# Optimization experiments

Measured on AMD Instinct MI355X. Metric: run time of the kernel, lower is better.

Reference implementation:

```python
import jax, jax.numpy as jnp
import numpy as np

D = 256
K = 64


def setup_inputs() -> dict:
    key = jax.random.key(0)
    k1, k2, k3 = jax.random.split(key, 3)
    B, H, W = 16, 96, 96
    X = jax.random.normal(k1, (B, D, H, W), dtype=jnp.float32)
    std1 = 1.0 / float(np.sqrt(K * D))
    std2 = 1.0 / float(np.sqrt(K))
    codewords = jax.random.uniform(k2, (K, D), dtype=jnp.float32, minval=-std1, maxval=std1)
    scale = jax.random.uniform(k3, (K,), dtype=jnp.float32, minval=-std2, maxval=std2)
    return {"X": X, "codewords": codewords, "scale": scale}


def reference(X, codewords, scale):
    # X: [B, D, H, W] -> Xf: [B, N, D]
    B = X.shape[0]
    Xf = X.reshape(B, X.shape[1], -1).transpose(0, 2, 1)
    # Scaled L2 distances: SL[b,n,k] = scale[k] * ||x_bn - c_k||^2
    x2 = jnp.sum(Xf * Xf, axis=-1, keepdims=True)          # [B, N, 1]
    c2 = jnp.sum(codewords * codewords, axis=-1)            # [K]
    xc = jnp.einsum('bnd,kd->bnk', Xf, codewords)           # [B, N, K]
    SL = scale * (x2 - 2.0 * xc + c2)                       # [B, N, K]
    # Assignment weights: softmax over codewords K
    A = jax.nn.softmax(SL, axis=-1)                         # [B, N, K]
    # Aggregate residuals: E[b,k,d] = sum_n A[b,n,k] * (X[b,n,d] - C[k,d])
    E = jnp.einsum('bnk,bnd->bkd', A, Xf) - jnp.sum(A, axis=1)[:, :, None] * codewords
    return E
```

## Files before the change

kernel.cpp:

```cpp
#include <hip/hip_runtime.h>

#define NDIM  256
#define NK    64
#define NPIX  9216
#define NB    16
#define TN    64
#define NW    48
#define TPB   3
#define GRID  (NB*NW)

typedef _Float16 half2_t __attribute__((ext_vector_type(2)));
typedef _Float16 half8_t __attribute__((ext_vector_type(8)));
typedef float    f32x4  __attribute__((ext_vector_type(4)));

__device__ __forceinline__ float fdot2(half2_t a, half2_t b, float c) {
  return __builtin_amdgcn_fdot2(a, b, c, false);
}

#define OFF_CH     0
#define OFF_C2     (NK * NDIM / 2)
#define OFF_ASUM   (OFF_C2 + NK)
#define OFF_APART  (OFF_ASUM + NB * NK)
#define OFF_EPART  (OFF_APART + GRID * NK)
#define WS_NEED    ((size_t)OFF_EPART * 4 + (size_t)GRID * NK * NDIM * 2)

__global__ void c2ch_kernel(const float* __restrict__ Cw, float* __restrict__ c2,
                            _Float16* __restrict__ ChH) {
  const int k = blockIdx.x, t = threadIdx.x;
  const float4 v = *(const float4*)(Cw + k * NDIM + 4 * t);
  half2_t h0; h0.x = (_Float16)v.x; h0.y = (_Float16)v.y;
  half2_t h1; h1.x = (_Float16)v.z; h1.y = (_Float16)v.w;
  *(half2_t*)&ChH[k * NDIM + 4 * t]     = h0;
  *(half2_t*)&ChH[k * NDIM + 4 * t + 2] = h1;
  float s = v.x*v.x + v.y*v.y + v.z*v.z + v.w*v.w;
#pragma unroll
  for (int o = 32; o; o >>= 1) s += __shfl_down(s, o);
  if (t == 0) c2[k] = s;
}

__global__ __launch_bounds__(256, 2) void encode_main(
    const float* __restrict__ X, const _Float16* __restrict__ ChH,
    const float* __restrict__ scale, const float* __restrict__ c2,
    void* __restrict__ Eout, float* __restrict__ Aout, int mode)
{
  __shared__ _Float16 XbS[32 * 66 * 8];
  __shared__ _Float16 Al[NK][72];
  __shared__ float red2[4][TN];
  __shared__ float redM[4][TN];
  __shared__ float redS[4][TN];

  const int tid  = threadIdx.x;
  const int w    = __builtin_amdgcn_readfirstlane(tid >> 6);
  const int lane = tid & 63;
  const int m    = lane & 15, quad = lane >> 4;
  const int b    = blockIdx.x / NW;
  const int wid  = blockIdx.x % NW;
  const float* Xbase = X + (size_t)b * NDIM * NPIX;
  const int kbase = w * 16;

  half8_t af1[8];
#pragma unroll
  for (int ks = 0; ks < 8; ++ks)
    af1[ks] = *(const half8_t*)(ChH + (kbase + m) * NDIM + ks * 32 + quad * 8);

  const float4 scv = *(const float4*)(scale + kbase + quad * 4);
  const float4 c2v = *(const float4*)(c2 + kbase + quad * 4);
  const float sc[4] = {scv.x, scv.y, scv.z, scv.w};
  const float sq[4] = {scv.x * c2v.x, scv.y * c2v.y, scv.z * c2v.z, scv.w * c2v.w};

  f32x4 acc_e[4][4];
#pragma unroll
  for (int i = 0; i < 4; ++i)
#pragma unroll
    for (int j = 0; j < 4; ++j)
      acc_e[i][j] = (f32x4){0.f, 0.f, 0.f, 0.f};
  float asum_acc = 0.f;

  float xv[64];
  {
    const float* Xg = Xbase + (size_t)(w * 64) * NPIX + wid * TN + lane;
#pragma unroll
    for (int i = 0; i < 64; ++i) xv[i] = Xg[(size_t)i * NPIX];
  }

  for (int tt = 0; tt < TPB; ++tt) {
    __syncthreads();

    {
      float xsq = 0.f;
#pragma unroll
      for (int g = 0; g < 8; ++g) {
        half8_t hv;
#pragma unroll
        for (int i = 0; i < 8; ++i) {
          const float v = xv[g * 8 + i];
          hv[i] = (_Float16)v; xsq += v * v;
        }
        *(half8_t*)&XbS[((w * 8 + g) * 66 + lane) * 8] = hv;
      }
      red2[w][lane] = xsq;
    }
    __syncthreads();

    if (tt + 1 < TPB) {
      const float* Xg = Xbase + (size_t)(w * 64) * NPIX + (wid + (tt + 1) * NW) * TN + lane;
#pragma unroll
      for (int i = 0; i < 64; ++i) xv[i] = Xg[(size_t)i * NPIX];
    }

    f32x4 accs[4];
#pragma unroll
    for (int nt = 0; nt < 4; ++nt) accs[nt] = (f32x4){0.f, 0.f, 0.f, 0.f};
#pragma unroll
    for (int ks = 0; ks < 8; ++ks) {
#pragma unroll
      for (int nt = 0; nt < 4; ++nt) {
        const half8_t bf = *(const half8_t*)&XbS[((ks * 4 + quad) * 66 + nt * 16 + m) * 8];
        accs[nt] = __builtin_amdgcn_mfma_f32_16x16x32_f16(af1[ks], bf, accs[nt], 0, 0, 0);
      }
    }

    float e[4][4], mw[4];
#pragma unroll
    for (int nt = 0; nt < 4; ++nt) {
      const int p = nt * 16 + m;
      const float x2p = red2[0][p] + red2[1][p] + red2[2][p] + red2[3][p];
      float L[4];
      float mx = -3.0e38f;
#pragma unroll
      for (int r = 0; r < 4; ++r) {
        L[r] = sc[r] * x2p - 2.f * sc[r] * accs[nt][r] + sq[r];
        mx = fmaxf(mx, L[r]);
      }
      mx = fmaxf(mx, __shfl_xor(mx, 16));
      mx = fmaxf(mx, __shfl_xor(mx, 32));
      float s = 0.f;
#pragma unroll
      for (int r = 0; r < 4; ++r) { e[nt][r] = __expf(L[r] - mx); s += e[nt][r]; }
      s += __shfl_xor(s, 16);
      s += __shfl_xor(s, 32);
      mw[nt] = mx;
      if (lane < 16) { redM[w][p] = mx; redS[w][p] = s; }
    }
    __syncthreads();
#pragma unroll
    for (int nt = 0; nt < 4; ++nt) {
      const int p = nt * 16 + m;
      const float M = fmaxf(fmaxf(redM[0][p], redM[1][p]),
                            fmaxf(redM[2][p], redM[3][p]));
      const float T = redS[0][p] * __expf(redM[0][p] - M)
                    + redS[1][p] * __expf(redM[1][p] - M)
                    + redS[2][p] * __expf(redM[2][p] - M)
                    + redS[3][p] * __expf(redM[3][p] - M);
      const float norm = __expf(mw[nt] - M) / T;
#pragma unroll
      for (int r = 0; r < 4; ++r)
        Al[kbase + quad * 4 + r][p] = (_Float16)(e[nt][r] * norm);
    }
    __syncthreads();

#pragma unroll
    for (int ks = 0; ks < 2; ++ks) {
      half8_t ba[4];
#pragma unroll
      for (int kt = 0; kt < 4; ++kt)
        ba[kt] = *(const half8_t*)&Al[kt * 16 + m][ks * 32 + quad * 8];
#pragma unroll
      for (int dt = 0; dt < 4; ++dt) {
        const int c = w * 8 + dt * 2 + (m >> 3);
        const int dlow = m & 7;
        half8_t xa;
#pragma unroll
        for (int j = 0; j < 8; ++j)
          xa[j] = XbS[(c * 66 + ks * 32 + quad * 8 + j) * 8 + dlow];
#pragma unroll
        for (int kt = 0; kt < 4; ++kt)
          acc_e[dt][kt] = __builtin_amdgcn_mfma_f32_16x16x32_f16(xa, ba[kt], acc_e[dt][kt], 0, 0, 0);
      }
    }
    if (tid < NK) {
      const half2_t one = {(_Float16)1.f, (_Float16)1.f};
#pragma unroll
      for (int lc = 0; lc < 8; ++lc) {
        const half8_t sv = *(const half8_t*)&Al[tid][lc * 8];
        asum_acc = fdot2(__builtin_shufflevector(sv, sv, 0, 1), one, asum_acc);
        asum_acc = fdot2(__builtin_shufflevector(sv, sv, 2, 3), one, asum_acc);
        asum_acc = fdot2(__builtin_shufflevector(sv, sv, 4, 5), one, asum_acc);
        asum_acc = fdot2(__builtin_shufflevector(sv, sv, 6, 7), one, asum_acc);
      }
    }
  }

  __syncthreads();
  _Float16* Et = XbS;
#pragma unroll
  for (int dt = 0; dt < 4; ++dt)
#pragma unroll
    for (int kt = 0; kt < 4; ++kt)
#pragma unroll
      for (int r = 0; r < 4; ++r) {
        const int k = kt * 16 + m;
        const int d = w * 64 + dt * 16 + quad * 4 + r;
        Et[k * 264 + d] = (_Float16)acc_e[dt][kt][r];
      }
  __syncthreads();
  const int ko = tid >> 2, cq = tid & 3;
  if (mode) {
    _Float16* Ebk = (_Float16*)Eout + (size_t)blockIdx.x * (NK * NDIM);
#pragma unroll
    for (int g = 0; g < 8; ++g)
      *(half8_t*)&Ebk[ko * NDIM + cq * 64 + g * 8] =
          *(const half8_t*)&Et[ko * 264 + cq * 64 + g * 8];
    if (tid < NK) Aout[blockIdx.x * NK + tid] = asum_acc;
  } else {
    float* Ebk = (float*)Eout + (size_t)b * (NK * NDIM);
#pragma unroll
    for (int g = 0; g < 64; ++g)
      atomicAdd(&Ebk[ko * NDIM + cq * 64 + g], (float)Et[ko * 264 + cq * 64 + g]);
    if (tid < NK) atomicAdd(&Aout[b * NK + tid], asum_acc);
  }
}

__global__ void asum_reduce_kernel(const float* __restrict__ Apart,
                                   float* __restrict__ asum) {
  const int i = blockIdx.x * 256 + threadIdx.x;
  const int bb = i >> 6, k = i & 63;
  float s = 0.f;
#pragma unroll 8
  for (int w = 0; w < NW; ++w) s += Apart[(bb * NW + w) * NK + k];
  asum[i] = s;
}

__global__ void finalize_partials(const _Float16* __restrict__ EpartH,
                                  const float* __restrict__ asum,
                                  const float* __restrict__ Cw,
                                  float* __restrict__ out) {
  const int g = blockIdx.x * 256 + threadIdx.x;
  const int i0 = g * 8;
  const int bb = i0 >> 14;
  const int o  = i0 & 16383;
  const int k  = o >> 8, d = i0 & 255;
  float s[8];
#pragma unroll
  for (int j = 0; j < 8; ++j) s[j] = 0.f;
  const _Float16* base = EpartH + (((size_t)bb * NW) << 14) + o;
#pragma unroll 4
  for (int w = 0; w < NW; ++w) {
    const half8_t v = *(const half8_t*)(base + ((size_t)w << 14));
#pragma unroll
    for (int j = 0; j < 8; ++j) s[j] += (float)v[j];
  }
  const float a = asum[bb * NK + k];
  const float4 c0 = *(const float4*)(Cw + k * NDIM + d);
  const float4 c1 = *(const float4*)(Cw + k * NDIM + d + 4);
  float4 r0, r1;
  r0.x = s[0] - a * c0.x; r0.y = s[1] - a * c0.y;
  r0.z = s[2] - a * c0.z; r0.w = s[3] - a * c0.w;
  r1.x = s[4] - a * c1.x; r1.y = s[5] - a * c1.y;
  r1.z = s[6] - a * c1.z; r1.w = s[7] - a * c1.w;
  *(float4*)(out + i0)     = r0;
  *(float4*)(out + i0 + 4) = r1;
}

__global__ void finalize_atomic(const float* __restrict__ E_acc,
                                const float* __restrict__ asum,
                                const float* __restrict__ Cw,
                                float* __restrict__ out) {
  const int i = blockIdx.x * 256 + threadIdx.x;
  const int d = i & 255;
  const int k = (i >> 8) & 63;
  const int bb = i >> 14;
  out[i] = E_acc[i] - asum[bb * NK + k] * Cw[k * NDIM + d];
}

extern "C" void kernel_launch(void* const* d_in, const int* in_sizes, int n_in,
                              void* d_out, int out_size, void* d_ws, size_t ws_size,
                              hipStream_t stream) {
  const float* X     = (const float*)d_in[0];
  const float* Cw    = (const float*)d_in[1];
  const float* scale = (const float*)d_in[2];
  float* out = (float*)d_out;

  float* wsf = (float*)d_ws;
  _Float16* ChH = (_Float16*)(wsf + OFF_CH);
  float* c2     = wsf + OFF_C2;
  float* asum   = wsf + OFF_ASUM;
  float* Apart  = wsf + OFF_APART;

  c2ch_kernel<<<NK, 64, 0, stream>>>(Cw, c2, ChH);
  if (ws_size >= WS_NEED) {
    _Float16* EpartH = (_Float16*)(wsf + OFF_EPART);
    encode_main<<<GRID, 256, 0, stream>>>(X, ChH, scale, c2, EpartH, Apart, 1);
    asum_reduce_kernel<<<4, 256, 0, stream>>>(Apart, asum);
    finalize_partials<<<(NB*NK*NDIM)/(256*8), 256, 0, stream>>>(EpartH, asum, Cw, out);
  } else {
    float* E_acc = wsf + OFF_APART;
    hipMemsetAsync(wsf + OFF_ASUM, 0,
                   (size_t)(NB*NK + GRID*NK + NB*NK*NDIM) * sizeof(float), stream);
    encode_main<<<GRID, 256, 0, stream>>>(X, ChH, scale, c2, E_acc, asum, 0);
    finalize_atomic<<<(NB*NK*NDIM)/256, 256, 0, stream>>>(E_acc, asum, Cw, out);
  }
}
```

Measured before the change: 243.0 us.

## Pre-convert X to fp16 tiled layout in a separate kernel before encoding

Adds a convert_x kernel that reads X once, writes an fp16 copy in the tiled LDS layout, and precomputes per-pixel squared norms. The main kernel then loads each tile with contiguous 16-byte loads instead of strided fp32 gathers and register prefetch. The assignment sums are now accumulated in registers from the fp32 softmax values rather than re-read from LDS. The cost is an extra kernel launch plus an extra global write and read of the fp16 X, about half the size of the original X. The LDS padding that avoided bank conflicts is also removed.

```diff
diff --git a/kernel.cpp b/kernel.cpp
--- a/kernel.cpp
+++ b/kernel.cpp
@@ -5,6 +5,7 @@
 #define NPIX  9216
 #define NB    16
 #define TN    64
+#define NTILE 144
 #define NW    48
 #define TPB   3
 #define GRID  (NB*NW)
@@ -21,8 +22,11 @@
 #define OFF_C2     (NK * NDIM / 2)
 #define OFF_ASUM   (OFF_C2 + NK)
 #define OFF_APART  (OFF_ASUM + NB * NK)
-#define OFF_EPART  (OFF_APART + GRID * NK)
-#define WS_NEED    ((size_t)OFF_EPART * 4 + (size_t)GRID * NK * NDIM * 2)
+#define OFF_X2     (OFF_APART + GRID * NK)
+#define OFF_XH     (OFF_X2 + NB * NPIX)
+#define XH_F       ((size_t)NB * NTILE * 32 * 64 * 8 / 2)
+#define OFF_EPART  ((size_t)OFF_XH + XH_F)
+#define WS_NEED    (OFF_EPART * 4 + (size_t)GRID * NK * NDIM * 2)
 
 __global__ void c2ch_kernel(const float* __restrict__ Cw, float* __restrict__ c2,
                             _Float16* __restrict__ ChH) {
@@ -38,16 +42,44 @@
   if (t == 0) c2[k] = s;
 }
 
-__global__ __launch_bounds__(256, 2) void encode_main(
-    const float* __restrict__ X, const _Float16* __restrict__ ChH,
-    const float* __restrict__ scale, const float* __restrict__ c2,
-    void* __restrict__ Eout, float* __restrict__ Aout, int mode)
+__global__ __launch_bounds__(256) void convert_x(
+    const float* __restrict__ X, _Float16* __restrict__ Xh,
+    float* __restrict__ x2g) {
+  __shared__ float red[4][TN];
+  const int tid = threadIdx.x;
+  const int w = tid >> 6, lane = tid & 63;
+  const int b = blockIdx.x / NTILE, tile = blockIdx.x % NTILE;
+  const int n0 = tile * TN;
+  const float* Xg = X + (size_t)b * NDIM * NPIX + (size_t)(w * 64) * NPIX + n0 + lane;
+  _Float16* dst = Xh + (size_t)(b * NTILE + tile) * (32 * 64 * 8);
+  float xsq = 0.f;
+#pragma unroll
+  for (int g = 0; g < 8; ++g) {
+    float v[8];
+#pragma unroll
+    for (int i = 0; i < 8; ++i) v[i] = Xg[(size_t)(g * 8 + i) * NPIX];
+    half8_t hv;
+#pragma unroll
+    for (int i = 0; i < 8; ++i) { hv[i] = (_Float16)v[i]; xsq += v[i] * v[i]; }
+    *(half8_t*)&dst[((w * 8 + g) * 64 + lane) * 8] = hv;
+  }
+  red[w][lane] = xsq;
+  __syncthreads();
+  if (tid < TN)
+    x2g[b * NPIX + n0 + tid] = red[0][tid] + red[1][tid] + red[2][tid] + red[3][tid];
+}
+
+__global__ __launch_bounds__(256, 2) void encode_b(
+    const _Float16* __restrict__ Xh, const float* __restrict__ x2g,
+    const _Float16* __restrict__ ChH, const float* __restrict__ scale,
+    const float* __restrict__ c2, void* __restrict__ Eout,
+    float* __restrict__ Aout, int mode)
 {
-  __shared__ _Float16 XbS[32 * 66 * 8];
-  __shared__ _Float16 Al[NK][72];
-  __shared__ float red2[4][TN];
-  __shared__ float redM[4][TN];
-  __shared__ float redS[4][TN];
+  __shared__ __align__(16) char smem[44032];
+  _Float16* XbS = (_Float16*)smem;
+  _Float16 (*Al)[72] = (_Float16(*)[72])(smem + 32768);
+  float* redM = (float*)(smem + 32768 + 9216);
+  float* redS = (float*)(smem + 32768 + 9216 + 1024);
 
   const int tid  = threadIdx.x;
   const int w    = __builtin_amdgcn_readfirstlane(tid >> 6);
@@ -55,7 +87,6 @@
   const int m    = lane & 15, quad = lane >> 4;
   const int b    = blockIdx.x / NW;
   const int wid  = blockIdx.x % NW;
-  const float* Xbase = X + (size_t)b * NDIM * NPIX;
   const int kbase = w * 16;
 
   half8_t af1[8];
@@ -74,40 +105,26 @@
 #pragma unroll
     for (int j = 0; j < 4; ++j)
       acc_e[i][j] = (f32x4){0.f, 0.f, 0.f, 0.f};
-  float asum_acc = 0.f;
-
-  float xv[64];
-  {
-    const float* Xg = Xbase + (size_t)(w * 64) * NPIX + wid * TN + lane;
-#pragma unroll
-    for (int i = 0; i < 64; ++i) xv[i] = Xg[(size_t)i * NPIX];
-  }
+  float asum_r[4] = {0.f, 0.f, 0.f, 0.f};
 
   for (int tt = 0; tt < TPB; ++tt) {
+    const int tile = wid + tt * NW;
+    const _Float16* src = Xh + (size_t)(b * NTILE + tile) * (32 * 64 * 8);
     __syncthreads();
 
-    {
-      float xsq = 0.f;
-#pragma unroll
-      for (int g = 0; g < 8; ++g) {
-        half8_t hv;
-#pragma unroll
-        for (int i = 0; i < 8; ++i) {
-          const float v = xv[g * 8 + i];
-          hv[i] = (_Float16)v; xsq += v * v;
-        }
-        *(half8_t*)&XbS[((w * 8 + g) * 66 + lane) * 8] = hv;
-      }
-      red2[w][lane] = xsq;
-    }
+    half8_t stg[8];
+#pragma unroll
+    for (int r = 0; r < 8; ++r)
+      stg[r] = *(const half8_t*)&src[(size_t)(tid + r * 256) * 8];
+    float x2v[4];
+#pragma unroll
+    for (int nt = 0; nt < 4; ++nt)
+      x2v[nt] = x2g[b * NPIX + tile * TN + nt * 16 + m];
+#pragma unroll
+    for (int r = 0; r < 8; ++r)
+      *(half8_t*)&XbS[(tid + r * 256) * 8] = stg[r];
     __syncthreads();
 
-    if (tt + 1 < TPB) {
-      const float* Xg = Xbase + (size_t)(w * 64) * NPIX + (wid + (tt + 1) * NW) * TN + lane;
-#pragma unroll
-      for (int i = 0; i < 64; ++i) xv[i] = Xg[(size_t)i * NPIX];
-    }
-
     f32x4 accs[4];
 #pragma unroll
     for (int nt = 0; nt < 4; ++nt) accs[nt] = (f32x4){0.f, 0.f, 0.f, 0.f};
@@ -115,7 +132,7 @@
     for (int ks = 0; ks < 8; ++ks) {
 #pragma unroll
       for (int nt = 0; nt < 4; ++nt) {
-        const half8_t bf = *(const half8_t*)&XbS[((ks * 4 + quad) * 66 + nt * 16 + m) * 8];
+        const half8_t bf = *(const half8_t*)&XbS[((ks * 4 + quad) * 64 + nt * 16 + m) * 8];
         accs[nt] = __builtin_amdgcn_mfma_f32_16x16x32_f16(af1[ks], bf, accs[nt], 0, 0, 0);
       }
     }
@@ -124,12 +141,11 @@
 #pragma unroll
     for (int nt = 0; nt < 4; ++nt) {
       const int p = nt * 16 + m;
-      const float x2p = red2[0][p] + red2[1][p] + red2[2][p] + red2[3][p];
       float L[4];
       float mx = -3.0e38f;
 #pragma unroll
       for (int r = 0; r < 4; ++r) {
-        L[r] = sc[r] * x2p - 2.f * sc[r] * accs[nt][r] + sq[r];
+        L[r] = sc[r] * x2v[nt] - 2.f * sc[r] * accs[nt][r] + sq[r];
         mx = fmaxf(mx, L[r]);
       }
       mx = fmaxf(mx, __shfl_xor(mx, 16));
@@ -140,22 +156,25 @@
       s += __shfl_xor(s, 16);
       s += __shfl_xor(s, 32);
       mw[nt] = mx;
-      if (lane < 16) { redM[w][p] = mx; redS[w][p] = s; }
+      if (lane < 16) { redM[w * 64 + p] = mx; redS[w * 64 + p] = s; }
     }
     __syncthreads();
 #pragma unroll
     for (int nt = 0; nt < 4; ++nt) {
       const int p = nt * 16 + m;
-      const float M = fmaxf(fmaxf(redM[0][p], redM[1][p]),
-                            fmaxf(redM[2][p], redM[3][p]));
-      const float T = redS[0][p] * __expf(redM[0][p] - M)
-                    + redS[1][p] * __expf(redM[1][p] - M)
-                    + redS[2][p] * __expf(redM[2][p] - M)
-                    + redS[3][p] * __expf(redM[3][p] - M);
+      const float M = fmaxf(fmaxf(redM[0 * 64 + p], redM[1 * 64 + p]),
+                            fmaxf(redM[2 * 64 + p], redM[3 * 64 + p]));
+      const float T = redS[0 * 64 + p] * __expf(redM[0 * 64 + p] - M)
+                    + redS[1 * 64 + p] * __expf(redM[1 * 64 + p] - M)
+                    + redS[2 * 64 + p] * __expf(redM[2 * 64 + p] - M)
+                    + redS[3 * 64 + p] * __expf(redM[3 * 64 + p] - M);
       const float norm = __expf(mw[nt] - M) / T;
 #pragma unroll
-      for (int r = 0; r < 4; ++r)
-        Al[kbase + quad * 4 + r][p] = (_Float16)(e[nt][r] * norm);
+      for (int r = 0; r < 4; ++r) {
+        const float a = e[nt][r] * norm;
+        Al[kbase + quad * 4 + r][p] = (_Float16)a;
+        asum_r[r] += a;
+      }
     }
     __syncthreads();
 
@@ -172,27 +191,16 @@
         half8_t xa;
 #pragma unroll
         for (int j = 0; j < 8; ++j)
-          xa[j] = XbS[(c * 66 + ks * 32 + quad * 8 + j) * 8 + dlow];
+          xa[j] = XbS[((c * 64 + ks * 32 + quad * 8 + j)) * 8 + dlow];
 #pragma unroll
         for (int kt = 0; kt < 4; ++kt)
           acc_e[dt][kt] = __builtin_amdgcn_mfma_f32_16x16x32_f16(xa, ba[kt], acc_e[dt][kt], 0, 0, 0);
       }
     }
-    if (tid < NK) {
-      const half2_t one = {(_Float16)1.f, (_Float16)1.f};
-#pragma unroll
-      for (int lc = 0; lc < 8; ++lc) {
-        const half8_t sv = *(const half8_t*)&Al[tid][lc * 8];
-        asum_acc = fdot2(__builtin_shufflevector(sv, sv, 0, 1), one, asum_acc);
-        asum_acc = fdot2(__builtin_shufflevector(sv, sv, 2, 3), one, asum_acc);
-        asum_acc = fdot2(__builtin_shufflevector(sv, sv, 4, 5), one, asum_acc);
-        asum_acc = fdot2(__builtin_shufflevector(sv, sv, 6, 7), one, asum_acc);
-      }
-    }
   }
 
   __syncthreads();
-  _Float16* Et = XbS;
+  _Float16* Et = (_Float16*)smem;
 #pragma unroll
   for (int dt = 0; dt < 4; ++dt)
 #pragma unroll
@@ -203,6 +211,12 @@
         const int d = w * 64 + dt * 16 + quad * 4 + r;
         Et[k * 264 + d] = (_Float16)acc_e[dt][kt][r];
       }
+#pragma unroll
+  for (int r = 0; r < 4; ++r) {
+#pragma unroll
+    for (int off = 1; off < 16; off <<= 1)
+      asum_r[r] += __shfl_xor(asum_r[r], off);
+  }
   __syncthreads();
   const int ko = tid >> 2, cq = tid & 3;
   if (mode) {
@@ -211,13 +225,19 @@
     for (int g = 0; g < 8; ++g)
       *(half8_t*)&Ebk[ko * NDIM + cq * 64 + g * 8] =
           *(const half8_t*)&Et[ko * 264 + cq * 64 + g * 8];
-    if (tid < NK) Aout[blockIdx.x * NK + tid] = asum_acc;
+    if (m == 0)
+#pragma unroll
+      for (int r = 0; r < 4; ++r)
+        Aout[blockIdx.x * NK + kbase + quad * 4 + r] = asum_r[r];
   } else {
     float* Ebk = (float*)Eout + (size_t)b * (NK * NDIM);
 #pragma unroll
     for (int g = 0; g < 64; ++g)
       atomicAdd(&Ebk[ko * NDIM + cq * 64 + g], (float)Et[ko * 264 + cq * 64 + g]);
-    if (tid < NK) atomicAdd(&Aout[b * NK + tid], asum_acc);
+    if (m == 0)
+#pragma unroll
+      for (int r = 0; r < 4; ++r)
+        atomicAdd(&Aout[b * NK + kbase + quad * 4 + r], asum_r[r]);
   }
 }
 
@@ -286,18 +306,21 @@
   float* c2     = wsf + OFF_C2;
   float* asum   = wsf + OFF_ASUM;
   float* Apart  = wsf + OFF_APART;
+  float* x2g    = wsf + OFF_X2;
+  _Float16* Xh  = (_Float16*)(wsf + OFF_XH);
 
   c2ch_kernel<<<NK, 64, 0, stream>>>(Cw, c2, ChH);
+  convert_x<<<NB * NTILE, 256, 0, stream>>>(X, Xh, x2g);
   if (ws_size >= WS_NEED) {
     _Float16* EpartH = (_Float16*)(wsf + OFF_EPART);
-    encode_main<<<GRID, 256, 0, stream>>>(X, ChH, scale, c2, EpartH, Apart, 1);
+    encode_b<<<GRID, 256, 0, stream>>>(Xh, x2g, ChH, scale, c2, EpartH, Apart, 1);
     asum_reduce_kernel<<<4, 256, 0, stream>>>(Apart, asum);
     finalize_partials<<<(NB*NK*NDIM)/(256*8), 256, 0, stream>>>(EpartH, asum, Cw, out);
   } else {
-    float* E_acc = wsf + OFF_APART;
-    hipMemsetAsync(wsf + OFF_ASUM, 0,
-                   (size_t)(NB*NK + GRID*NK + NB*NK*NDIM) * sizeof(float), stream);
-    encode_main<<<GRID, 256, 0, stream>>>(X, ChH, scale, c2, E_acc, asum, 0);
+    float* E_acc = (float*)(wsf + OFF_EPART);
+    hipMemsetAsync(asum, 0, (size_t)(NB*NK) * sizeof(float), stream);
+    hipMemsetAsync(E_acc, 0, (size_t)(NB*NK*NDIM) * sizeof(float), stream);
+    encode_b<<<GRID, 256, 0, stream>>>(Xh, x2g, ChH, scale, c2, E_acc, asum, 0);
     finalize_atomic<<<(NB*NK*NDIM)/256, 256, 0, stream>>>(E_acc, asum, Cw, out);
   }
 }
```

Result: slower. 280.0 us (+15.3%).
